# Optimization experiments

Measured on AMD Instinct MI355X. Metric: run time of the kernel, lower is better.

## Reference

```python
import jax, jax.numpy as jnp
import numpy as np
import math

HIDDEN = 1024
NUM_HEADS = 16
NUM_GROUPS = 16  # source einsum/rearrange only shape-checks when groups == heads
HEAD_DIM = HIDDEN // NUM_HEADS


def rope(x, base=10000.0):
    # x: [b, s, d]; applied to the FULL hidden vector before head split, as in source.
    # Source rope_fn has a reshape bug; this is the intended rotate-half RoPE with
    # half_d frequencies 1/base^(i/half_d) (== 1/base^(2i/d)).
    b, s, d = x.shape
    half = d // 2
    x1, x2 = x[..., :half], x[..., half:]
    pos = jnp.arange(s, dtype=x.dtype)[:, None]                          # [s,1]
    inv_freq = 1.0 / (base ** (jnp.arange(half, dtype=x.dtype) / half))  # [half]
    ang = pos * inv_freq[None, :]                                        # [s,half]
    sin = jnp.sin(ang)[None]                                             # [1,s,half]
    cos = jnp.cos(ang)[None]
    return jnp.concatenate([x1 * cos - x2 * sin, x2 * cos + x1 * sin], axis=-1)


def setup_inputs() -> dict:
    key = jax.random.key(0)
    ks = jax.random.split(key, 10)
    scale = 1.0 / math.sqrt(HIDDEN)
    inp = {
        "x": jax.random.normal(ks[0], (2, 2048, HIDDEN), dtype=jnp.float32),
        "attn_mask": jax.random.randint(ks[1], (2, 2048), 0, 2, dtype=jnp.int32),
        "Wq": jax.random.uniform(ks[2], (HIDDEN, HIDDEN), jnp.float32, -scale, scale),
        "bq": jax.random.uniform(ks[3], (HIDDEN,), jnp.float32, -scale, scale),
        "Wk": jax.random.uniform(ks[4], (HIDDEN, HIDDEN), jnp.float32, -scale, scale),
        "bk": jax.random.uniform(ks[5], (HIDDEN,), jnp.float32, -scale, scale),
        "Wv": jax.random.uniform(ks[6], (HIDDEN, HIDDEN), jnp.float32, -scale, scale),
        "bv": jax.random.uniform(ks[7], (HIDDEN,), jnp.float32, -scale, scale),
        "Wo": jax.random.uniform(ks[8], (HIDDEN, HIDDEN), jnp.float32, -scale, scale),
        "bo": jax.random.uniform(ks[9], (HIDDEN,), jnp.float32, -scale, scale),
    }
    return inp


def reference(x, attn_mask, Wq, bq, Wk, bk, Wv, bv, Wo, bo):
    b, s, _ = x.shape
    g = NUM_GROUPS
    subh = NUM_HEADS // g  # = 1 here
    d = HIDDEN // g        # per-group dim (== head dim when g == h)

    q = rope(x @ Wq.T + bq)
    k = rope(x @ Wk.T + bk)
    v = x @ Wv.T + bv

    # q: b s (g subh d) -> b g subh s d ; k,v: b s (g d) -> b g s d
    q = q.reshape(b, s, g, subh, d).transpose(0, 2, 3, 1, 4)
    k = k.reshape(b, s, g, d).transpose(0, 2, 1, 3)
    v = v.reshape(b, s, g, d).transpose(0, 2, 1, 3)

    e = jnp.einsum('bghqd,bgkd->bghqk', q, k) / math.sqrt(HEAD_DIM)  # [b,g,subh,s,s]
    mask5 = attn_mask[:, None, None, None, :]  # broadcast over g, subh, query
    e = jnp.where(mask5 == 0, -jnp.inf, e)
    attn = jax.nn.softmax(e, axis=-1)
    out = jnp.einsum('bghqk,bgkd->bghqd', attn, v)            # [b,g,subh,s,d]
    out = out.transpose(0, 3, 1, 2, 4).reshape(b, s, HIDDEN)  # b s (g subh d)
    return out @ Wo.T + bo
```

## Files before the change

### kernel.cpp

```cpp
#include <hip/hip_runtime.h>
#include <hip/hip_bf16.h>


constexpr int Bb  = 2;
constexpr int Ss  = 2048;
constexpr int Hh  = 1024;
constexpr int NHh = 16;
constexpr int Mm  = Bb * Ss;

typedef __attribute__((ext_vector_type(8))) unsigned short ushort8;
typedef __attribute__((ext_vector_type(4))) unsigned short ushort4_t;
typedef __attribute__((ext_vector_type(8))) short short8;
typedef __attribute__((ext_vector_type(4))) float f32x4;

__device__ __forceinline__ unsigned short f2bf(float f) {
    unsigned int u = __float_as_uint(f);
    u += 0x7fffu + ((u >> 16) & 1u);
    return (unsigned short)(u >> 16);
}
__device__ __forceinline__ float bf2f(unsigned short h) {
    return __uint_as_float(((unsigned int)h) << 16);
}
__device__ __forceinline__ void gload16(const void* g, void* l) {
    __builtin_amdgcn_global_load_lds(
        (const __attribute__((address_space(1))) unsigned int*)g,
        (__attribute__((address_space(3))) unsigned int*)l, 16, 0, 0);
}

__global__ __launch_bounds__(256) void convert_k(
    const float* __restrict__ x,
    const float* __restrict__ Wq, const float* __restrict__ Wk,
    const float* __restrict__ Wv, const float* __restrict__ Wo,
    unsigned short* __restrict__ xb, unsigned short* __restrict__ wall)
{
    size_t e = ((size_t)blockIdx.x * 256 + threadIdx.x) << 3;
    const float* s; unsigned short* d;
    if (e < (size_t)Mm * Hh) {
        s = x + e; d = xb + e;
    } else {
        size_t f = e - (size_t)Mm * Hh;
        int t = (int)(f >> 20);
        const float* w = (t == 0) ? Wq : (t == 1) ? Wk : (t == 2) ? Wv : Wo;
        s = w + (f & 1048575);
        d = wall + f;
    }
    float4 a = *(const float4*)s;
    float4 b = *(const float4*)(s + 4);
    ushort8 o;
    o[0] = f2bf(a.x); o[1] = f2bf(a.y); o[2] = f2bf(a.z); o[3] = f2bf(a.w);
    o[4] = f2bf(b.x); o[5] = f2bf(b.y); o[6] = f2bf(b.z); o[7] = f2bf(b.w);
    *(ushort8*)d = o;
}

#define GEMM_BODY(ATYPE_PTR, WPTR, K0MAX)                                          \
    __shared__ unsigned short As[128 * 64];                                        \
    __shared__ unsigned short Bs[128 * 64];                                        \
    const int tid  = threadIdx.x;                                                  \
    const int lane = tid & 63;                                                     \
    const int w    = tid >> 6;                                                     \
    const int wr   = w >> 1, wc = w & 1;                                           \
    const int l16  = lane & 15, g = lane >> 4;                                     \
    const int R0   = blockIdx.x * 128;                                             \
    char* asb = (char*)As; char* bsb = (char*)Bs;                                  \
    f32x4 acc[4][4] = {};                                                          \
    for (int k0 = 0; k0 < K0MAX; k0 += 64) {                                       \
        _Pragma("unroll")                                                          \
        for (int it = 0; it < 4; ++it) {                                           \
            int sbase = w * 4096 + it * 1024;                                      \
            int boff  = sbase + lane * 16;                                         \
            int r     = boff >> 7;                                                 \
            int c     = (boff >> 4) & 7;                                           \
            int col   = k0 + ((c ^ (r & 7)) << 3);                                 \
            gload16(&ATYPE_PTR[(size_t)(R0 + r) * 1024 + col], asb + sbase);       \
            gload16(&WPTR[(size_t)(gn + r) * 1024 + col], bsb + sbase);            \
        }                                                                          \
        __syncthreads();                                                           \
        short8 bfrag[4][2];                                                        \
        _Pragma("unroll")                                                          \
        for (int u = 0; u < 4; ++u) {                                              \
            int row = wc * 64 + u * 16 + l16;                                      \
            _Pragma("unroll")                                                      \
            for (int s = 0; s < 2; ++s)                                            \
                bfrag[u][s] = *(const short8*)(bsb + row * 128 +                   \
                               ((s * 64 + g * 16) ^ ((row & 7) << 4)));            \
        }                                                                          \
        _Pragma("unroll")                                                          \
        for (int t = 0; t < 4; ++t) {                                              \
            int row = wr * 64 + t * 16 + l16;                                      \
            short8 af[2];                                                          \
            _Pragma("unroll")                                                      \
            for (int s = 0; s < 2; ++s)                                            \
                af[s] = *(const short8*)(asb + row * 128 +                         \
                         ((s * 64 + g * 16) ^ ((row & 7) << 4)));                  \
            _Pragma("unroll")                                                      \
            for (int u = 0; u < 4; ++u) {                                          \
                acc[t][u] = __builtin_amdgcn_mfma_f32_16x16x32_bf16(af[0], bfrag[u][0], acc[t][u], 0, 0, 0); \
                acc[t][u] = __builtin_amdgcn_mfma_f32_16x16x32_bf16(af[1], bfrag[u][1], acc[t][u], 0, 0, 0); \
            }                                                                      \
        }                                                                          \
        __syncthreads();                                                           \
    }

__global__ __launch_bounds__(256) void gemm_qkv_k(
    const unsigned short* __restrict__ xb, const unsigned short* __restrict__ wall,
    const float* __restrict__ bq, const float* __restrict__ bk, const float* __restrict__ bv,
    unsigned short* __restrict__ q, unsigned short* __restrict__ k2,
    unsigned short* __restrict__ v)
{
    const int gn = blockIdx.y * 128;
    GEMM_BODY(xb, wall, 1024)

    const int sel = gn >> 10;
    const int n0  = gn & 1023;
    const float* bias = (sel == 0) ? bq : (sel == 1) ? bk : bv;
    unsigned short* outp = (sel == 0) ? q : (sel == 1) ? k2 : v;
    #pragma unroll
    for (int u = 0; u < 4; ++u) {
        int coll = wc * 64 + u * 16 + l16;
        float bb = bias[n0 + coll];
        #pragma unroll
        for (int t = 0; t < 4; ++t)
            #pragma unroll
            for (int rr = 0; rr < 4; ++rr) {
                int row = R0 + wr * 64 + t * 16 + g * 4 + rr;
                outp[(size_t)row * 1024 + n0 + coll] = f2bf(acc[t][u][rr] + bb);
            }
    }
}

__global__ __launch_bounds__(256) void gemm_out_k(
    const unsigned short* __restrict__ ao, const unsigned short* __restrict__ wo,
    const float* __restrict__ bo, float* __restrict__ out)
{
    const int gn = blockIdx.y * 128;
    GEMM_BODY(ao, wo, 1024)

    #pragma unroll
    for (int u = 0; u < 4; ++u) {
        int coll = wc * 64 + u * 16 + l16;
        float bb = bo[gn + coll];
        #pragma unroll
        for (int t = 0; t < 4; ++t)
            #pragma unroll
            for (int rr = 0; rr < 4; ++rr) {
                int row = R0 + wr * 64 + t * 16 + g * 4 + rr;
                out[(size_t)row * 1024 + gn + coll] = acc[t][u][rr] + bb;
            }
    }
}

__global__ __launch_bounds__(256) void rope_k(
    unsigned short* __restrict__ q, unsigned short* __restrict__ kk)
{
    int idx = blockIdx.x * 256 + threadIdx.x;
    int row = idx >> 7;
    int j4  = (idx & 127) << 2;
    int pos = row & (Ss - 1);
    size_t base = (size_t)row * 1024;

    ushort4_t qa = *(ushort4_t*)&q[base + j4];
    ushort4_t qb = *(ushort4_t*)&q[base + 512 + j4];
    ushort4_t ka = *(ushort4_t*)&kk[base + j4];
    ushort4_t kb = *(ushort4_t*)&kk[base + 512 + j4];

    #pragma unroll
    for (int t = 0; t < 4; ++t) {
        float jj = (float)(j4 + t);
        float inv = exp2f(jj * -0.0259525632621414f);
        float ang = (float)pos * inv;
        float sn, cs;
        __sincosf(ang, &sn, &cs);
        float a = bf2f(qa[t]), b = bf2f(qb[t]);
        qa[t] = f2bf(a * cs - b * sn);
        qb[t] = f2bf(b * cs + a * sn);
        float c = bf2f(ka[t]), d = bf2f(kb[t]);
        ka[t] = f2bf(c * cs - d * sn);
        kb[t] = f2bf(d * cs + c * sn);
    }
    *(ushort4_t*)&q[base + j4]        = qa;
    *(ushort4_t*)&q[base + 512 + j4]  = qb;
    *(ushort4_t*)&kk[base + j4]       = ka;
    *(ushort4_t*)&kk[base + 512 + j4] = kb;
}

__global__ __launch_bounds__(256) void flash_k(
    const unsigned short* __restrict__ q, const unsigned short* __restrict__ k,
    const unsigned short* __restrict__ v, const int* __restrict__ mask,
    unsigned short* __restrict__ ao)
{
    __shared__ unsigned short Ks[64 * 64];
    __shared__ unsigned short Vt[64 * 64];
    __shared__ unsigned short Pb[4][32 * 64];

    const int F   = blockIdx.x + 16 * blockIdx.y + 256 * blockIdx.z;
    const int xcd = F & 7, j = F >> 3;
    const int grp = xcd + 8 * (j >> 4);
    const int qb  = j & 15;
    const int h   = grp & 15;
    const int bz  = grp >> 4;

    const int tid  = threadIdx.x;
    const int lane = tid & 63;
    const int w    = tid >> 6;
    const int l16  = lane & 15;
    const int g    = lane >> 4;
    const int sw   = (lane & 7) << 4;

    char* ksb = (char*)&Ks[0];
    char* vtb = (char*)&Vt[0];
    char* pbb = (char*)&Pb[w][0];

    const int qrowbase = bz * Ss + qb * 128 + w * 32;

    short8 qf[2][2];
    #pragma unroll
    for (int t = 0; t < 2; ++t)
        #pragma unroll
        for (int s = 0; s < 2; ++s)
            qf[t][s] = *(const short8*)&q[(size_t)(qrowbase + t * 16 + l16) * 1024
                                          + h * 64 + s * 32 + g * 8];

    f32x4 O[2][4];
    #pragma unroll
    for (int t = 0; t < 2; ++t)
        #pragma unroll
        for (int d = 0; d < 4; ++d) O[t][d] = (f32x4)0.f;
    f32x4 Osum[2];
    Osum[0] = (f32x4)0.f; Osum[1] = (f32x4)0.f;
    float mrow[2] = {-1e30f, -1e30f};

    const float SCALE = 0.18033688011112042f;
    const float THR   = 10.0f;

    short8 ones;
    #pragma unroll
    for (int e = 0; e < 8; ++e) ones[e] = (short)0x3F80;

    for (int kt = 0; kt < Ss / 64; ++kt) {
        #pragma unroll
        for (int it = 0; it < 2; ++it) {
            int cid = w * 128 + it * 64 + lane;
            int row = cid >> 3;
            int sub = cid & 7;
            gload16(&k[(size_t)(bz * Ss + kt * 64 + row) * 1024 + h * 64
                       + ((sub ^ (row & 7)) << 3)],
                    ksb + w * 2048 + it * 1024);
        }
        {
            int kv    = tid & 63;
            int dbase = (tid >> 6) << 4;
            #pragma unroll
            for (int half = 0; half < 2; ++half) {
                int d0 = dbase + half * 8;
                ushort8 t8 = *(const ushort8*)&v[(size_t)(bz * Ss + kt * 64 + kv) * 1024
                                                 + h * 64 + d0];
                #pragma unroll
                for (int jj = 0; jj < 8; ++jj) {
                    int d = d0 + jj;
                    *(unsigned short*)(vtb + d * 128 + ((kv * 2) ^ ((d & 7) << 4))) = t8[jj];
                }
            }
        }
        __syncthreads();

        f32x4 S[2][4];
        #pragma unroll
        for (int t = 0; t < 2; ++t)
            #pragma unroll
            for (int kt4 = 0; kt4 < 4; ++kt4) S[t][kt4] = (f32x4)0.f;

        #pragma unroll
        for (int kt4 = 0; kt4 < 4; ++kt4) {
            int key = kt4 * 16 + l16;
            short8 kf0 = *(const short8*)(ksb + key * 128 + ((g * 16) ^ sw));
            short8 kf1 = *(const short8*)(ksb + key * 128 + ((64 + g * 16) ^ sw));
            #pragma unroll
            for (int t = 0; t < 2; ++t) {
                S[t][kt4] = __builtin_amdgcn_mfma_f32_16x16x32_bf16(kf0, qf[t][0], S[t][kt4], 0, 0, 0);
                S[t][kt4] = __builtin_amdgcn_mfma_f32_16x16x32_bf16(kf1, qf[t][1], S[t][kt4], 0, 0, 0);
            }
        }

        int mk[4][4];
        #pragma unroll
        for (int kt4 = 0; kt4 < 4; ++kt4)
            *(int4*)&mk[kt4][0] = *(const int4*)&mask[bz * Ss + kt * 64 + kt4 * 16 + g * 4];
        #pragma unroll
        for (int t = 0; t < 2; ++t)
            #pragma unroll
            for (int kt4 = 0; kt4 < 4; ++kt4)
                #pragma unroll
                for (int r = 0; r < 4; ++r)
                    S[t][kt4][r] = mk[kt4][r] ? S[t][kt4][r] * SCALE : -1e30f;

        float rm[2];
        #pragma unroll
        for (int t = 0; t < 2; ++t) {
            float m01 = fmaxf(fmaxf(S[t][0][0], S[t][0][1]), fmaxf(S[t][0][2], S[t][0][3]));
            float m23 = fmaxf(fmaxf(S[t][1][0], S[t][1][1]), fmaxf(S[t][1][2], S[t][1][3]));
            float m45 = fmaxf(fmaxf(S[t][2][0], S[t][2][1]), fmaxf(S[t][2][2], S[t][2][3]));
            float m67 = fmaxf(fmaxf(S[t][3][0], S[t][3][1]), fmaxf(S[t][3][2], S[t][3][3]));
            float m = fmaxf(fmaxf(m01, m23), fmaxf(m45, m67));
            m = fmaxf(m, __shfl_xor(m, 16));
            m = fmaxf(m, __shfl_xor(m, 32));
            rm[t] = m;
        }

        bool grow = (rm[0] > mrow[0] + THR) || (rm[1] > mrow[1] + THR);
        if (__any((int)grow)) {
            float mn0 = fmaxf(mrow[0], rm[0]);
            float mn1 = fmaxf(mrow[1], rm[1]);
            float rs0 = exp2f(mrow[0] - mn0);
            float rs1 = exp2f(mrow[1] - mn1);
            mrow[0] = mn0; mrow[1] = mn1;
            #pragma unroll
            for (int r = 0; r < 4; ++r) {
                float f0 = __shfl(rs0, g * 4 + r);
                float f1 = __shfl(rs1, g * 4 + r);
                #pragma unroll
                for (int dt = 0; dt < 4; ++dt) { O[0][dt][r] *= f0; O[1][dt][r] *= f1; }
                Osum[0][r] *= f0; Osum[1][r] *= f1;
            }
        }

        #pragma unroll
        for (int t = 0; t < 2; ++t)
            #pragma unroll
            for (int kt4 = 0; kt4 < 4; ++kt4) {
                float p0 = exp2f(S[t][kt4][0] - mrow[t]);
                float p1 = exp2f(S[t][kt4][1] - mrow[t]);
                float p2 = exp2f(S[t][kt4][2] - mrow[t]);
                float p3 = exp2f(S[t][kt4][3] - mrow[t]);
                unsigned int u01, u23;
                asm("v_cvt_pk_bf16_f32 %0, %1, %2" : "=v"(u01) : "v"(p0), "v"(p1));
                asm("v_cvt_pk_bf16_f32 %0, %1, %2" : "=v"(u23) : "v"(p2), "v"(p3));
                int prow = t * 16 + l16;
                int pbyte = (kt4 * 32 + g * 8) ^ ((prow & 7) << 4);
                *(uint2*)(pbb + prow * 128 + pbyte) = make_uint2(u01, u23);
            }

        #pragma unroll
        for (int ks = 0; ks < 2; ++ks) {
            short8 pf0 = *(const short8*)(pbb + l16 * 128 + ((ks * 64 + g * 16) ^ sw));
            short8 pf1 = *(const short8*)(pbb + (16 + l16) * 128 + ((ks * 64 + g * 16) ^ sw));
            Osum[0] = __builtin_amdgcn_mfma_f32_16x16x32_bf16(pf0, ones, Osum[0], 0, 0, 0);
            Osum[1] = __builtin_amdgcn_mfma_f32_16x16x32_bf16(pf1, ones, Osum[1], 0, 0, 0);
            #pragma unroll
            for (int dt = 0; dt < 4; ++dt) {
                short8 vf = *(const short8*)(vtb + (dt * 16 + l16) * 128 + ((ks * 64 + g * 16) ^ sw));
                O[0][dt] = __builtin_amdgcn_mfma_f32_16x16x32_bf16(pf0, vf, O[0][dt], 0, 0, 0);
                O[1][dt] = __builtin_amdgcn_mfma_f32_16x16x32_bf16(pf1, vf, O[1][dt], 0, 0, 0);
            }
        }
        __syncthreads();
    }

    #pragma unroll
    for (int t = 0; t < 2; ++t)
        #pragma unroll
        for (int r = 0; r < 4; ++r) {
            float inv = 1.0f / Osum[t][r];
            int row = qrowbase + t * 16 + g * 4 + r;
            #pragma unroll
            for (int dt = 0; dt < 4; ++dt)
                ao[(size_t)row * 1024 + h * 64 + dt * 16 + l16] = f2bf(O[t][dt][r] * inv);
        }
}

extern "C" void kernel_launch(void* const* d_in, const int* in_sizes, int n_in,
                              void* d_out, int out_size, void* d_ws, size_t ws_size,
                              hipStream_t stream)
{
    const float* x  = (const float*)d_in[0];
    const int*   am = (const int*)d_in[1];
    const float* Wq = (const float*)d_in[2];
    const float* bq = (const float*)d_in[3];
    const float* Wk = (const float*)d_in[4];
    const float* bk = (const float*)d_in[5];
    const float* Wv = (const float*)d_in[6];
    const float* bv = (const float*)d_in[7];
    const float* Wo = (const float*)d_in[8];
    const float* bo = (const float*)d_in[9];
    float* out = (float*)d_out;

    const size_t NE = (size_t)Mm * Hh;
    unsigned short* q    = (unsigned short*)d_ws;
    unsigned short* k    = q + NE;
    unsigned short* v    = k + NE;
    unsigned short* ao   = v + NE;
    unsigned short* xb   = ao + NE;
    unsigned short* wall = xb + NE;
    unsigned short* wo   = wall + 3u * 1048576u;

    convert_k<<<(2 * NE) / (256 * 8), 256, 0, stream>>>(x, Wq, Wk, Wv, Wo, xb, wall);
    gemm_qkv_k<<<dim3(Mm / 128, 3072 / 128), 256, 0, stream>>>(
        xb, wall, bq, bk, bv, q, k, v);
    rope_k<<<(Mm * 128) / 256, 256, 0, stream>>>(q, k);
    flash_k<<<dim3(Ss / 128, NHh, Bb), 256, 0, stream>>>(q, k, v, am, ao);
    gemm_out_k<<<dim3(Mm / 128, Hh / 128), 256, 0, stream>>>(ao, wo, bo, out);
}
```

Before: 171.3 us.

## Halve flash query tile per wave and fold softmax scale into Q

The flash attention kernel now gives each wave 16 query rows instead of 32, so each block covers 64 queries and the grid doubles to 1024 one-dimensional blocks with an XCD-aware remap. Fewer accumulator registers and launch_bounds(256,4) are meant to raise occupancy. The softmax scale is applied to Q in the QKV GEMM epilogue, and RoPE, being linear, keeps that scale. This removes the per-score multiply. The cost is that each block reuses its loaded K/V tile across half as many queries, so global and LDS traffic per unit of work doubles.

Result: no change. 168.2 us (-1.9%).

```diff
diff --git a/kernel.cpp b/kernel.cpp
--- a/kernel.cpp
+++ b/kernel.cpp
@@ -114,6 +114,7 @@
     const int n0  = gn & 1023;
     const float* bias = (sel == 0) ? bq : (sel == 1) ? bk : bv;
     unsigned short* outp = (sel == 0) ? q : (sel == 1) ? k2 : v;
+    const float qs = (sel == 0) ? 0.18033688011112042f : 1.0f;
     #pragma unroll
     for (int u = 0; u < 4; ++u) {
         int coll = wc * 64 + u * 16 + l16;
@@ -123,7 +124,7 @@
             #pragma unroll
             for (int rr = 0; rr < 4; ++rr) {
                 int row = R0 + wr * 64 + t * 16 + g * 4 + rr;
-                outp[(size_t)row * 1024 + n0 + coll] = f2bf(acc[t][u][rr] + bb);
+                outp[(size_t)row * 1024 + n0 + coll] = f2bf((acc[t][u][rr] + bb) * qs);
             }
     }
 }
@@ -183,19 +184,19 @@
     *(ushort4_t*)&kk[base + 512 + j4] = kb;
 }
 
-__global__ __launch_bounds__(256) void flash_k(
+__global__ __launch_bounds__(256, 4) void flash_k(
     const unsigned short* __restrict__ q, const unsigned short* __restrict__ k,
     const unsigned short* __restrict__ v, const int* __restrict__ mask,
     unsigned short* __restrict__ ao)
 {
     __shared__ unsigned short Ks[64 * 64];
     __shared__ unsigned short Vt[64 * 64];
-    __shared__ unsigned short Pb[4][32 * 64];
-
-    const int F   = blockIdx.x + 16 * blockIdx.y + 256 * blockIdx.z;
+    __shared__ unsigned short Pb[4][16 * 64];
+
+    const int F   = blockIdx.x;
     const int xcd = F & 7, j = F >> 3;
-    const int grp = xcd + 8 * (j >> 4);
-    const int qb  = j & 15;
+    const int grp = xcd * 4 + (j >> 5);
+    const int qb  = j & 31;
     const int h   = grp & 15;
     const int bz  = grp >> 4;
 
@@ -210,27 +211,21 @@
     char* vtb = (char*)&Vt[0];
     char* pbb = (char*)&Pb[w][0];
 
-    const int qrowbase = bz * Ss + qb * 128 + w * 32;
-
-    short8 qf[2][2];
-    #pragma unroll
-    for (int t = 0; t < 2; ++t)
-        #pragma unroll
-        for (int s = 0; s < 2; ++s)
-            qf[t][s] = *(const short8*)&q[(size_t)(qrowbase + t * 16 + l16) * 1024
-                                          + h * 64 + s * 32 + g * 8];
-
-    f32x4 O[2][4];
-    #pragma unroll
-    for (int t = 0; t < 2; ++t)
-        #pragma unroll
-        for (int d = 0; d < 4; ++d) O[t][d] = (f32x4)0.f;
-    f32x4 Osum[2];
-    Osum[0] = (f32x4)0.f; Osum[1] = (f32x4)0.f;
-    float mrow[2] = {-1e30f, -1e30f};
-
-    const float SCALE = 0.18033688011112042f;
-    const float THR   = 10.0f;
+    const int qrowbase = bz * Ss + qb * 64 + w * 16;
+
+    short8 qf[2];
+    #pragma unroll
+    for (int s = 0; s < 2; ++s)
+        qf[s] = *(const short8*)&q[(size_t)(qrowbase + l16) * 1024
+                                   + h * 64 + s * 32 + g * 8];
+
+    f32x4 O[4];
+    #pragma unroll
+    for (int d = 0; d < 4; ++d) O[d] = (f32x4)0.f;
+    f32x4 Osum = (f32x4)0.f;
+    float mrow = -1.0e4f;
+
+    const float THR = 10.0f;
 
     short8 ones;
     #pragma unroll
@@ -263,22 +258,16 @@
         }
         __syncthreads();
 
-        f32x4 S[2][4];
-        #pragma unroll
-        for (int t = 0; t < 2; ++t)
-            #pragma unroll
-            for (int kt4 = 0; kt4 < 4; ++kt4) S[t][kt4] = (f32x4)0.f;
-
+        f32x4 S[4];
+        #pragma unroll
+        for (int kt4 = 0; kt4 < 4; ++kt4) S[kt4] = (f32x4)0.f;
         #pragma unroll
         for (int kt4 = 0; kt4 < 4; ++kt4) {
             int key = kt4 * 16 + l16;
             short8 kf0 = *(const short8*)(ksb + key * 128 + ((g * 16) ^ sw));
             short8 kf1 = *(const short8*)(ksb + key * 128 + ((64 + g * 16) ^ sw));
-            #pragma unroll
-            for (int t = 0; t < 2; ++t) {
-                S[t][kt4] = __builtin_amdgcn_mfma_f32_16x16x32_bf16(kf0, qf[t][0], S[t][kt4], 0, 0, 0);
-                S[t][kt4] = __builtin_amdgcn_mfma_f32_16x16x32_bf16(kf1, qf[t][1], S[t][kt4], 0, 0, 0);
-            }
+            S[kt4] = __builtin_amdgcn_mfma_f32_16x16x32_bf16(kf0, qf[0], S[kt4], 0, 0, 0);
+            S[kt4] = __builtin_amdgcn_mfma_f32_16x16x32_bf16(kf1, qf[1], S[kt4], 0, 0, 0);
         }
 
         int mk[4][4];
@@ -286,85 +275,66 @@
         for (int kt4 = 0; kt4 < 4; ++kt4)
             *(int4*)&mk[kt4][0] = *(const int4*)&mask[bz * Ss + kt * 64 + kt4 * 16 + g * 4];
         #pragma unroll
-        for (int t = 0; t < 2; ++t)
-            #pragma unroll
-            for (int kt4 = 0; kt4 < 4; ++kt4)
+        for (int kt4 = 0; kt4 < 4; ++kt4)
+            #pragma unroll
+            for (int r = 0; r < 4; ++r)
+                S[kt4][r] = mk[kt4][r] ? S[kt4][r] : -1e30f;
+
+        float m0 = fmaxf(fmaxf(S[0][0], S[0][1]), fmaxf(S[0][2], S[0][3]));
+        float m1 = fmaxf(fmaxf(S[1][0], S[1][1]), fmaxf(S[1][2], S[1][3]));
+        float m2 = fmaxf(fmaxf(S[2][0], S[2][1]), fmaxf(S[2][2], S[2][3]));
+        float m3 = fmaxf(fmaxf(S[3][0], S[3][1]), fmaxf(S[3][2], S[3][3]));
+        float m  = fmaxf(fmaxf(m0, m1), fmaxf(m2, m3));
+        m = fmaxf(m, __shfl_xor(m, 16));
+        m = fmaxf(m, __shfl_xor(m, 32));
+
+        if (__any((int)(m > mrow + THR))) {
+            float mn = fmaxf(mrow, m);
+            float rs = exp2f(mrow - mn);
+            mrow = mn;
+            #pragma unroll
+            for (int r = 0; r < 4; ++r) {
+                float f0 = __shfl(rs, g * 4 + r);
                 #pragma unroll
-                for (int r = 0; r < 4; ++r)
-                    S[t][kt4][r] = mk[kt4][r] ? S[t][kt4][r] * SCALE : -1e30f;
-
-        float rm[2];
-        #pragma unroll
-        for (int t = 0; t < 2; ++t) {
-            float m01 = fmaxf(fmaxf(S[t][0][0], S[t][0][1]), fmaxf(S[t][0][2], S[t][0][3]));
-            float m23 = fmaxf(fmaxf(S[t][1][0], S[t][1][1]), fmaxf(S[t][1][2], S[t][1][3]));
-            float m45 = fmaxf(fmaxf(S[t][2][0], S[t][2][1]), fmaxf(S[t][2][2], S[t][2][3]));
-            float m67 = fmaxf(fmaxf(S[t][3][0], S[t][3][1]), fmaxf(S[t][3][2], S[t][3][3]));
-            float m = fmaxf(fmaxf(m01, m23), fmaxf(m45, m67));
-            m = fmaxf(m, __shfl_xor(m, 16));
-            m = fmaxf(m, __shfl_xor(m, 32));
-            rm[t] = m;
-        }
-
-        bool grow = (rm[0] > mrow[0] + THR) || (rm[1] > mrow[1] + THR);
-        if (__any((int)grow)) {
-            float mn0 = fmaxf(mrow[0], rm[0]);
-            float mn1 = fmaxf(mrow[1], rm[1]);
-            float rs0 = exp2f(mrow[0] - mn0);
-            float rs1 = exp2f(mrow[1] - mn1);
-            mrow[0] = mn0; mrow[1] = mn1;
-            #pragma unroll
-            for (int r = 0; r < 4; ++r) {
-                float f0 = __shfl(rs0, g * 4 + r);
-                float f1 = __shfl(rs1, g * 4 + r);
-                #pragma unroll
-                for (int dt = 0; dt < 4; ++dt) { O[0][dt][r] *= f0; O[1][dt][r] *= f1; }
-                Osum[0][r] *= f0; Osum[1][r] *= f1;
-            }
-        }
-
-        #pragma unroll
-        for (int t = 0; t < 2; ++t)
-            #pragma unroll
-            for (int kt4 = 0; kt4 < 4; ++kt4) {
-                float p0 = exp2f(S[t][kt4][0] - mrow[t]);
-                float p1 = exp2f(S[t][kt4][1] - mrow[t]);
-                float p2 = exp2f(S[t][kt4][2] - mrow[t]);
-                float p3 = exp2f(S[t][kt4][3] - mrow[t]);
-                unsigned int u01, u23;
-                asm("v_cvt_pk_bf16_f32 %0, %1, %2" : "=v"(u01) : "v"(p0), "v"(p1));
-                asm("v_cvt_pk_bf16_f32 %0, %1, %2" : "=v"(u23) : "v"(p2), "v"(p3));
-                int prow = t * 16 + l16;
-                int pbyte = (kt4 * 32 + g * 8) ^ ((prow & 7) << 4);
-                *(uint2*)(pbb + prow * 128 + pbyte) = make_uint2(u01, u23);
-            }
+                for (int dt = 0; dt < 4; ++dt) O[dt][r] *= f0;
+                Osum[r] *= f0;
+            }
+        }
+
+        #pragma unroll
+        for (int kt4 = 0; kt4 < 4; ++kt4) {
+            float p0 = exp2f(S[kt4][0] - mrow);
+            float p1 = exp2f(S[kt4][1] - mrow);
+            float p2 = exp2f(S[kt4][2] - mrow);
+            float p3 = exp2f(S[kt4][3] - mrow);
+            unsigned int u01, u23;
+            asm("v_cvt_pk_bf16_f32 %0, %1, %2" : "=v"(u01) : "v"(p0), "v"(p1));
+            asm("v_cvt_pk_bf16_f32 %0, %1, %2" : "=v"(u23) : "v"(p2), "v"(p3));
+            int pbyte = (kt4 * 32 + g * 8) ^ ((l16 & 7) << 4);
+            *(uint2*)(pbb + l16 * 128 + pbyte) = make_uint2(u01, u23);
+        }
 
         #pragma unroll
         for (int ks = 0; ks < 2; ++ks) {
-            short8 pf0 = *(const short8*)(pbb + l16 * 128 + ((ks * 64 + g * 16) ^ sw));
-            short8 pf1 = *(const short8*)(pbb + (16 + l16) * 128 + ((ks * 64 + g * 16) ^ sw));
-            Osum[0] = __builtin_amdgcn_mfma_f32_16x16x32_bf16(pf0, ones, Osum[0], 0, 0, 0);
-            Osum[1] = __builtin_amdgcn_mfma_f32_16x16x32_bf16(pf1, ones, Osum[1], 0, 0, 0);
+            short8 pf = *(const short8*)(pbb + l16 * 128 + ((ks * 64 + g * 16) ^ sw));
+            Osum = __builtin_amdgcn_mfma_f32_16x16x32_bf16(pf, ones, Osum, 0, 0, 0);
             #pragma unroll
             for (int dt = 0; dt < 4; ++dt) {
                 short8 vf = *(const short8*)(vtb + (dt * 16 + l16) * 128 + ((ks * 64 + g * 16) ^ sw));
-                O[0][dt] = __builtin_amdgcn_mfma_f32_16x16x32_bf16(pf0, vf, O[0][dt], 0, 0, 0);
-                O[1][dt] = __builtin_amdgcn_mfma_f32_16x16x32_bf16(pf1, vf, O[1][dt], 0, 0, 0);
+                O[dt] = __builtin_amdgcn_mfma_f32_16x16x32_bf16(pf, vf, O[dt], 0, 0, 0);
             }
         }
         __syncthreads();
     }
 
     #pragma unroll
-    for (int t = 0; t < 2; ++t)
-        #pragma unroll
-        for (int r = 0; r < 4; ++r) {
-            float inv = 1.0f / Osum[t][r];
-            int row = qrowbase + t * 16 + g * 4 + r;
-            #pragma unroll
-            for (int dt = 0; dt < 4; ++dt)
-                ao[(size_t)row * 1024 + h * 64 + dt * 16 + l16] = f2bf(O[t][dt][r] * inv);
-        }
+    for (int r = 0; r < 4; ++r) {
+        float inv = 1.0f / Osum[r];
+        int row = qrowbase + g * 4 + r;
+        #pragma unroll
+        for (int dt = 0; dt < 4; ++dt)
+            ao[(size_t)row * 1024 + h * 64 + dt * 16 + l16] = f2bf(O[dt][r] * inv);
+    }
 }
 
 extern "C" void kernel_launch(void* const* d_in, const int* in_sizes, int n_in,
@@ -396,6 +366,6 @@
     gemm_qkv_k<<<dim3(Mm / 128, 3072 / 128), 256, 0, stream>>>(
         xb, wall, bq, bk, bv, q, k, v);
     rope_k<<<(Mm * 128) / 256, 256, 0, stream>>>(q, k);
-    flash_k<<<dim3(Ss / 128, NHh, Bb), 256, 0, stream>>>(q, k, v, am, ao);
+    flash_k<<<dim3(Ss / 64 * NHh * Bb), 256, 0, stream>>>(q, k, v, am, ao);
     gemm_out_k<<<dim3(Mm / 128, Hh / 128), 256, 0, stream>>>(ao, wo, bo, out);
 }
```

## Double-buffer K/V tiles in flash attention and fold softmax scale into Q

Applied to the files above, without the earlier changes.

The flash kernel now double-buffers the K and V shared-memory tiles, issuing global loads for the next key tile before computing the current one. The V transpose write is deferred until after the PV MFMAs, so one barrier per iteration is enough. V is stored in a padded (stride 72) layout instead of an XOR swizzle. The softmax scale (including log2e) is folded into Q at the QKV GEMM epilogue, which removes the per-score multiply. The grid is flattened with a new XCD-aware block mapping, and launch bounds now request 3 blocks per CU, which raises shared memory use and register pressure.

Measured after the change: 164.4 us. 4.0% less time.

```diff
diff --git a/kernel.cpp b/kernel.cpp
--- a/kernel.cpp
+++ b/kernel.cpp
@@ -114,6 +114,7 @@
     const int n0  = gn & 1023;
     const float* bias = (sel == 0) ? bq : (sel == 1) ? bk : bv;
     unsigned short* outp = (sel == 0) ? q : (sel == 1) ? k2 : v;
+    const float qs = (sel == 0) ? 0.18033688011112042f : 1.0f;
     #pragma unroll
     for (int u = 0; u < 4; ++u) {
         int coll = wc * 64 + u * 16 + l16;
@@ -123,7 +124,7 @@
             #pragma unroll
             for (int rr = 0; rr < 4; ++rr) {
                 int row = R0 + wr * 64 + t * 16 + g * 4 + rr;
-                outp[(size_t)row * 1024 + n0 + coll] = f2bf(acc[t][u][rr] + bb);
+                outp[(size_t)row * 1024 + n0 + coll] = f2bf((acc[t][u][rr] + bb) * qs);
             }
     }
 }
@@ -183,18 +184,18 @@
     *(ushort4_t*)&kk[base + 512 + j4] = kb;
 }
 
-__global__ __launch_bounds__(256) void flash_k(
+__global__ __launch_bounds__(256, 3) void flash_k(
     const unsigned short* __restrict__ q, const unsigned short* __restrict__ k,
     const unsigned short* __restrict__ v, const int* __restrict__ mask,
     unsigned short* __restrict__ ao)
 {
-    __shared__ unsigned short Ks[64 * 64];
-    __shared__ unsigned short Vt[64 * 64];
+    __shared__ unsigned short Ks[2][64 * 64];
+    __shared__ unsigned short Vt[2][64 * 72];
     __shared__ unsigned short Pb[4][32 * 64];
 
-    const int F   = blockIdx.x + 16 * blockIdx.y + 256 * blockIdx.z;
+    const int F   = blockIdx.x;
     const int xcd = F & 7, j = F >> 3;
-    const int grp = xcd + 8 * (j >> 4);
+    const int grp = xcd * 4 + (j >> 4);
     const int qb  = j & 15;
     const int h   = grp & 15;
     const int bz  = grp >> 4;
@@ -206,11 +207,8 @@
     const int g    = lane >> 4;
     const int sw   = (lane & 7) << 4;
 
-    char* ksb = (char*)&Ks[0];
-    char* vtb = (char*)&Vt[0];
-    char* pbb = (char*)&Pb[w][0];
-
     const int qrowbase = bz * Ss + qb * 128 + w * 32;
+    const size_t kvbase = (size_t)(bz * Ss) * 1024 + h * 64;
 
     short8 qf[2][2];
     #pragma unroll
@@ -227,48 +225,60 @@
         for (int d = 0; d < 4; ++d) O[t][d] = (f32x4)0.f;
     f32x4 Osum[2];
     Osum[0] = (f32x4)0.f; Osum[1] = (f32x4)0.f;
-    float mrow[2] = {-1e30f, -1e30f};
-
-    const float SCALE = 0.18033688011112042f;
-    const float THR   = 10.0f;
+    float mrow[2] = {-1.0e4f, -1.0e4f};
+
+    const float THR = 10.0f;
 
     short8 ones;
     #pragma unroll
     for (int e = 0; e < 8; ++e) ones[e] = (short)0x3F80;
 
+    const int kv    = lane;
+    const int dbase = w * 16;
+
+    ushort8 vr0 = *(const ushort8*)&v[kvbase + (size_t)kv * 1024 + dbase];
+    ushort8 vr1 = *(const ushort8*)&v[kvbase + (size_t)kv * 1024 + dbase + 8];
+    #pragma unroll
+    for (int it = 0; it < 2; ++it) {
+        int cid = w * 128 + it * 64 + lane;
+        int row = cid >> 3;
+        int sub = cid & 7;
+        gload16(&k[kvbase + (size_t)row * 1024 + ((sub ^ (row & 7)) << 3)],
+                (char*)&Ks[0][0] + w * 2048 + it * 1024);
+    }
+    #pragma unroll
+    for (int jj = 0; jj < 8; ++jj) {
+        Vt[0][(dbase + jj) * 72 + kv]     = vr0[jj];
+        Vt[0][(dbase + 8 + jj) * 72 + kv] = vr1[jj];
+    }
+    __syncthreads();
+
     for (int kt = 0; kt < Ss / 64; ++kt) {
-        #pragma unroll
-        for (int it = 0; it < 2; ++it) {
-            int cid = w * 128 + it * 64 + lane;
-            int row = cid >> 3;
-            int sub = cid & 7;
-            gload16(&k[(size_t)(bz * Ss + kt * 64 + row) * 1024 + h * 64
-                       + ((sub ^ (row & 7)) << 3)],
-                    ksb + w * 2048 + it * 1024);
-        }
-        {
-            int kv    = tid & 63;
-            int dbase = (tid >> 6) << 4;
-            #pragma unroll
-            for (int half = 0; half < 2; ++half) {
-                int d0 = dbase + half * 8;
-                ushort8 t8 = *(const ushort8*)&v[(size_t)(bz * Ss + kt * 64 + kv) * 1024
-                                                 + h * 64 + d0];
-                #pragma unroll
-                for (int jj = 0; jj < 8; ++jj) {
-                    int d = d0 + jj;
-                    *(unsigned short*)(vtb + d * 128 + ((kv * 2) ^ ((d & 7) << 4))) = t8[jj];
-                }
-            }
-        }
-        __syncthreads();
+        const int cur = kt & 1;
+        char* ksb = (char*)&Ks[cur][0];
+        char* vtb = (char*)&Vt[cur][0];
+        char* pbb = (char*)&Pb[w][0];
+        const bool pre = (kt + 1 < Ss / 64);
+
+        if (pre) {
+            size_t nb = kvbase + (size_t)(kt + 1) * 64 * 1024;
+            vr0 = *(const ushort8*)&v[nb + (size_t)kv * 1024 + dbase];
+            vr1 = *(const ushort8*)&v[nb + (size_t)kv * 1024 + dbase + 8];
+            #pragma unroll
+            for (int it = 0; it < 2; ++it) {
+                int cid = w * 128 + it * 64 + lane;
+                int row = cid >> 3;
+                int sub = cid & 7;
+                gload16(&k[nb + (size_t)row * 1024 + ((sub ^ (row & 7)) << 3)],
+                        (char*)&Ks[cur ^ 1][0] + w * 2048 + it * 1024);
+            }
+        }
 
         f32x4 S[2][4];
         #pragma unroll
         for (int t = 0; t < 2; ++t)
             #pragma unroll
             for (int kt4 = 0; kt4 < 4; ++kt4) S[t][kt4] = (f32x4)0.f;
-
         #pragma unroll
         for (int kt4 = 0; kt4 < 4; ++kt4) {
             int key = kt4 * 16 + l16;
@@ -291,16 +301,16 @@
             for (int kt4 = 0; kt4 < 4; ++kt4)
                 #pragma unroll
                 for (int r = 0; r < 4; ++r)
-                    S[t][kt4][r] = mk[kt4][r] ? S[t][kt4][r] * SCALE : -1e30f;
+                    S[t][kt4][r] = mk[kt4][r] ? S[t][kt4][r] : -1e30f;
 
         float rm[2];
         #pragma unroll
         for (int t = 0; t < 2; ++t) {
-            float m01 = fmaxf(fmaxf(S[t][0][0], S[t][0][1]), fmaxf(S[t][0][2], S[t][0][3]));
-            float m23 = fmaxf(fmaxf(S[t][1][0], S[t][1][1]), fmaxf(S[t][1][2], S[t][1][3]));
-            float m45 = fmaxf(fmaxf(S[t][2][0], S[t][2][1]), fmaxf(S[t][2][2], S[t][2][3]));
-            float m67 = fmaxf(fmaxf(S[t][3][0], S[t][3][1]), fmaxf(S[t][3][2], S[t][3][3]));
-            float m = fmaxf(fmaxf(m01, m23), fmaxf(m45, m67));
+            float m0 = fmaxf(fmaxf(S[t][0][0], S[t][0][1]), fmaxf(S[t][0][2], S[t][0][3]));
+            float m1 = fmaxf(fmaxf(S[t][1][0], S[t][1][1]), fmaxf(S[t][1][2], S[t][1][3]));
+            float m2 = fmaxf(fmaxf(S[t][2][0], S[t][2][1]), fmaxf(S[t][2][2], S[t][2][3]));
+            float m3 = fmaxf(fmaxf(S[t][3][0], S[t][3][1]), fmaxf(S[t][3][2], S[t][3][3]));
+            float m  = fmaxf(fmaxf(m0, m1), fmaxf(m2, m3));
             m = fmaxf(m, __shfl_xor(m, 16));
             m = fmaxf(m, __shfl_xor(m, 32));
             rm[t] = m;
@@ -324,7 +334,8 @@
         }
 
         #pragma unroll
-        for (int t = 0; t < 2; ++t)
+        for (int t = 0; t < 2; ++t) {
+            int prow = t * 16 + l16;
             #pragma unroll
             for (int kt4 = 0; kt4 < 4; ++kt4) {
                 float p0 = exp2f(S[t][kt4][0] - mrow[t]);
@@ -334,22 +345,33 @@
                 unsigned int u01, u23;
                 asm("v_cvt_pk_bf16_f32 %0, %1, %2" : "=v"(u01) : "v"(p0), "v"(p1));
                 asm("v_cvt_pk_bf16_f32 %0, %1, %2" : "=v"(u23) : "v"(p2), "v"(p3));
-                int prow = t * 16 + l16;
-                int pbyte = (kt4 * 32 + g * 8) ^ ((prow & 7) << 4);
+                int pbyte = (kt4 * 32 + g * 8) ^ sw;
                 *(uint2*)(pbb + prow * 128 + pbyte) = make_uint2(u01, u23);
             }
+        }
 
         #pragma unroll
         for (int ks = 0; ks < 2; ++ks) {
-            short8 pf0 = *(const short8*)(pbb + l16 * 128 + ((ks * 64 + g * 16) ^ sw));
-            short8 pf1 = *(const short8*)(pbb + (16 + l16) * 128 + ((ks * 64 + g * 16) ^ sw));
-            Osum[0] = __builtin_amdgcn_mfma_f32_16x16x32_bf16(pf0, ones, Osum[0], 0, 0, 0);
-            Osum[1] = __builtin_amdgcn_mfma_f32_16x16x32_bf16(pf1, ones, Osum[1], 0, 0, 0);
+            short8 pf[2];
+            #pragma unroll
+            for (int t = 0; t < 2; ++t)
+                pf[t] = *(const short8*)(pbb + (t * 16 + l16) * 128 + ((ks * 64 + g * 16) ^ sw));
+            Osum[0] = __builtin_amdgcn_mfma_f32_16x16x32_bf16(pf[0], ones, Osum[0], 0, 0, 0);
+            Osum[1] = __builtin_amdgcn_mfma_f32_16x16x32_bf16(pf[1], ones, Osum[1], 0, 0, 0);
             #pragma unroll
             for (int dt = 0; dt < 4; ++dt) {
-                short8 vf = *(const short8*)(vtb + (dt * 16 + l16) * 128 + ((ks * 64 + g * 16) ^ sw));
-                O[0][dt] = __builtin_amdgcn_mfma_f32_16x16x32_bf16(pf0, vf, O[0][dt], 0, 0, 0);
-                O[1][dt] = __builtin_amdgcn_mfma_f32_16x16x32_bf16(pf1, vf, O[1][dt], 0, 0, 0);
+                short8 vf = *(const short8*)((const char*)vtb
+                              + ((dt * 16 + l16) * 72 + ks * 32 + g * 8) * 2);
+                O[0][dt] = __builtin_amdgcn_mfma_f32_16x16x32_bf16(pf[0], vf, O[0][dt], 0, 0, 0);
+                O[1][dt] = __builtin_amdgcn_mfma_f32_16x16x32_bf16(pf[1], vf, O[1][dt], 0, 0, 0);
+            }
+        }
+
+        if (pre) {
+            #pragma unroll
+            for (int jj = 0; jj < 8; ++jj) {
+                Vt[cur ^ 1][(dbase + jj) * 72 + kv]     = vr0[jj];
+                Vt[cur ^ 1][(dbase + 8 + jj) * 72 + kv] = vr1[jj];
             }
         }
         __syncthreads();
@@ -396,6 +418,6 @@
     gemm_qkv_k<<<dim3(Mm / 128, 3072 / 128), 256, 0, stream>>>(
         xb, wall, bq, bk, bv, q, k, v);
     rope_k<<<(Mm * 128) / 256, 256, 0, stream>>>(q, k);
-    flash_k<<<dim3(Ss / 128, NHh, Bb), 256, 0, stream>>>(q, k, v, am, ao);
+    flash_k<<<dim3(Ss / 128 * NHh * Bb), 256, 0, stream>>>(q, k, v, am, ao);
     gemm_out_k<<<dim3(Mm / 128, Hh / 128), 256, 0, stream>>>(ao, wo, bo, out);
 }
```
